# Kernel tuning notes

Hardware: AMD Instinct MI355X
Metric: run time of the kernel (lower is better)

## Reference

```python
import jax, jax.numpy as jnp
import numpy as np

B, S, H, V = 2, 2048, 1024, 32000
SDS = [64, 128, 256]
EPS = 1e-5


def _ln(x, g, b):
    m = jnp.mean(x, -1, keepdims=True)
    v = jnp.var(x, -1, keepdims=True)
    return (x - m) * jax.lax.rsqrt(v + EPS) * g + b


def _layer(x, A_log, Wb, Wc, D, Wg, bg, Wo, bo, g, be):
    # x: [B,S,H]; state dim N = A_log.shape[0]
    A = jnp.exp(A_log)
    gate = jax.nn.sigmoid(jnp.einsum('bsh,nh->bsn', x, Wg) + bg)
    Bx = jnp.einsum('bsh,nh->bsn', x, Wb)
    u = gate * Bx  # [B,S,N]

    def step(s, u_t):
        s = A * s + u_t
        return s, s

    s0 = jnp.zeros((x.shape[0], A.shape[0]), x.dtype)
    _, states = jax.lax.scan(step, s0, jnp.swapaxes(u, 0, 1))  # [S,B,N]
    states = jnp.swapaxes(states, 0, 1)
    y = jnp.einsum('bsn,hn->bsh', states, Wc) + D * x
    out = _ln(y + x, g, be)
    return out @ Wo.T + bo  # dropout is identity (p used in eval / p=0)


def setup_inputs() -> dict:
    key = jax.random.key(0)
    ks = iter(jax.random.split(key, 64))
    d = {}
    d['x'] = jax.random.randint(next(ks), (B, S), 0, V)
    d['E'] = jax.random.normal(next(ks), (V, H), jnp.float32) * 0.02
    for i, N in enumerate(SDS):
        d[f'A{i}'] = jnp.log(jnp.exp(jnp.full((N,), -0.5)) + 0.1 * jax.random.normal(next(ks), (N,)))
        d[f'Wb{i}'] = jax.random.normal(next(ks), (N, H), jnp.float32) * 0.02
        d[f'Wc{i}'] = jax.random.normal(next(ks), (H, N), jnp.float32) * 0.02
        d[f'D{i}'] = jax.random.normal(next(ks), (H,), jnp.float32)
        d[f'Wg{i}'] = jax.random.normal(next(ks), (N, H), jnp.float32) * 0.02
        d[f'bg{i}'] = jnp.zeros((N,), jnp.float32)
        d[f'Wo{i}'] = jax.random.normal(next(ks), (H, H), jnp.float32) * 0.02
        d[f'bo{i}'] = jnp.zeros((H,), jnp.float32)
        d[f'g{i}'] = jnp.ones((H,), jnp.float32)
        d[f'be{i}'] = jnp.zeros((H,), jnp.float32)
    d['Wf'] = jax.random.normal(next(ks), (H, 3 * H), jnp.float32) * 0.02
    d['bf'] = jnp.zeros((H,), jnp.float32)
    d['gf'] = jnp.ones((H,), jnp.float32)
    d['bef'] = jnp.zeros((H,), jnp.float32)
    d['Wh'] = jax.random.normal(next(ks), (V, H), jnp.float32) * 0.02
    d['bh'] = jnp.zeros((V,), jnp.float32)
    return d


def reference(x, E,
              A0, Wb0, Wc0, D0, Wg0, bg0, Wo0, bo0, g0, be0,
              A1, Wb1, Wc1, D1, Wg1, bg1, Wo1, bo1, g1, be1,
              A2, Wb2, Wc2, D2, Wg2, bg2, Wo2, bo2, g2, be2,
              Wf, bf, gf, bef, Wh, bh):
    emb = E[x]  # [B,S,H]
    o0 = _layer(emb, A0, Wb0, Wc0, D0, Wg0, bg0, Wo0, bo0, g0, be0)
    o1 = _layer(emb, A1, Wb1, Wc1, D1, Wg1, bg1, Wo1, bo1, g1, be1)
    o2 = _layer(emb, A2, Wb2, Wc2, D2, Wg2, bg2, Wo2, bo2, g2, be2)
    combined = jnp.concatenate([o0, o1, o2], axis=-1)  # [B,S,3H]
    fused = combined @ Wf.T + bf
    fused = _ln(fused + emb, gf, bef)
    logits = fused @ Wh.T + bh  # [B,S,V]
    return logits
```

## Files before the change

### kernel.cpp

```cpp
#include <hip/hip_runtime.h>
#include <hip/hip_bf16.h>

#define Hd 1024
#define Bdim 2
#define Sd 2048
#define BSd 4096
#define Vd 32000
#define EPSf 1e-5f
#define CH 16
#define NCH 128
#define NT3 448

typedef __attribute__((ext_vector_type(8))) short short8;
typedef __attribute__((ext_vector_type(4))) float f32x4;
typedef __attribute__((ext_vector_type(4))) unsigned short us4;

__device__ __forceinline__ unsigned short f2bf(float f) {
  union { float f; unsigned int u; } v; v.f = f;
  return (unsigned short)((v.u + 0x7fffu + ((v.u >> 16) & 1u)) >> 16);
}

typedef __attribute__((address_space(1))) const void gvoid_t;
typedef __attribute__((address_space(3))) void svoid_t;
__device__ __forceinline__ void gl_lds16(const void* g, void* s) {
  __builtin_amdgcn_global_load_lds((gvoid_t*)g, (svoid_t*)s, 16, 0, 0);
}

struct CvtTab {
  const float* src[11];
  unsigned short* dst[11];
  int start[12];
};
__global__ void k_cvt_all(CvtTab tab) {
  int b = blockIdx.x;
  int j = 0;
  while (j < 10 && b >= tab.start[j + 1]) ++j;
  size_t i = (size_t)(b - tab.start[j]) * 256 + threadIdx.x;
  f32x4 v = *(const f32x4*)(tab.src[j] + i * 4);
  us4 o;
  o[0] = f2bf(v[0]); o[1] = f2bf(v[1]); o[2] = f2bf(v[2]); o[3] = f2bf(v[3]);
  *(us4*)(tab.dst[j] + i * 4) = o;
}

__global__ void k_cvtT(const float* __restrict__ s0, const float* __restrict__ s1,
                       const float* __restrict__ s2, unsigned short* __restrict__ dst) {
  const float* src = blockIdx.z == 0 ? s0 : (blockIdx.z == 1 ? s1 : s2);
  unsigned short* d = dst + (size_t)blockIdx.z * Hd * Hd;
  __shared__ float tile[32][33];
  int tx = threadIdx.x & 31, ty = threadIdx.x >> 5;
  int bx = blockIdx.x * 32, by = blockIdx.y * 32;
  #pragma unroll
  for (int i = 0; i < 4; ++i)
    tile[ty + i * 8][tx] = src[(size_t)(by + ty + i * 8) * Hd + bx + tx];
  __syncthreads();
  #pragma unroll
  for (int i = 0; i < 4; ++i)
    d[(size_t)(bx + ty + i * 8) * Hd + by + tx] = f2bf(tile[tx][ty + i * 8]);
}

__global__ void k_biasf(const float* __restrict__ Wf_, const float* __restrict__ bfb,
                        const float* __restrict__ bo0, const float* __restrict__ bo1,
                        const float* __restrict__ bo2, float* __restrict__ biasf) {
  int h = blockIdx.x, t = threadIdx.x;
  float s = 0.f;
  for (int c = t; c < 3072; c += 256) {
    float b = c < 1024 ? bo0[c] : (c < 2048 ? bo1[c - 1024] : bo2[c - 2048]);
    s += Wf_[(size_t)h * 3072 + c] * b;
  }
  #pragma unroll
  for (int o = 32; o >= 1; o >>= 1) s += __shfl_xor(s, o);
  __shared__ float red[4];
  if ((t & 63) == 0) red[t >> 6] = s;
  __syncthreads();
  if (t == 0) biasf[h] = bfb[h] + red[0] + red[1] + red[2] + red[3];
}

__global__ void k_setup(const float* A0, const float* A1, const float* A2,
                        const float* b0, const float* b1, const float* b2,
                        const float* D0, const float* D1, const float* D2,
                        const float* g0, const float* g1, const float* g2,
                        const float* e0, const float* e1, const float* e2,
                        float* Alog448, float* bg448,
                        float* D3, float* g3, float* be3) {
  int t = blockIdx.x * 256 + threadIdx.x;
  if (t < NT3) {
    int l = t < 64 ? 0 : (t < 192 ? 1 : 2);
    int o = t - (l == 0 ? 0 : (l == 1 ? 64 : 192));
    Alog448[t] = (l == 0 ? A0 : (l == 1 ? A1 : A2))[o];
    bg448[t]   = (l == 0 ? b0 : (l == 1 ? b1 : b2))[o];
  }
  if (t < 3072) {
    int l = t >> 10, o = t & 1023;
    D3[t]  = (l == 0 ? D0 : (l == 1 ? D1 : D2))[o];
    g3[t]  = (l == 0 ? g0 : (l == 1 ? g1 : g2))[o];
    be3[t] = (l == 0 ? e0 : (l == 1 ? e1 : e2))[o];
  }
}

__global__ void k_embed(const int* __restrict__ x, const float* __restrict__ E,
                        float* __restrict__ emb, unsigned short* __restrict__ embbf) {
  int row = blockIdx.x, t = threadIdx.x;
  int id = x[row];
  f32x4 v = *(const f32x4*)(E + (size_t)id * Hd + t * 4);
  *(f32x4*)(emb + (size_t)row * Hd + t * 4) = v;
  us4 o;
  o[0] = f2bf(v[0]); o[1] = f2bf(v[1]); o[2] = f2bf(v[2]); o[3] = f2bf(v[3]);
  *(us4*)(embbf + (size_t)row * Hd + t * 4) = o;
}

template<int BM, int BN, int WM, int WN, int BF16_OUT>
__launch_bounds__(WM * WN * 64)
__global__ void gemm2ph(const unsigned short* __restrict__ A,
                        const unsigned short* __restrict__ Bw,
                        const float* __restrict__ bias,
                        void* __restrict__ Cv,
                        int N, int K, int lda, int ldb, int ldc, int coff, int tm)
{
  constexpr int NT = WM * WN * 64;
  constexpr int MF = BM / WM / 16;
  constexpr int NF = BN / WN / 16;
  constexpr int ASZ = BM * 64;
  constexpr int BSZ = BN * 64;
  constexpr int AR = (ASZ * 2) / (NT * 16);
  constexpr int BR = (BSZ * 2) / (NT * 16);
  __shared__ __align__(16) unsigned short Sm[2 * (ASZ + BSZ)];

  int T = gridDim.x;
  int orig = blockIdx.x;
  int q = T >> 3, r = T & 7;
  int xc = orig & 7, sdv = orig >> 3;
  int wgid = (xc < r ? xc * (q + 1) : r * (q + 1) + (xc - r) * q) + sdv;
  int n_t = wgid / tm, m_t = wgid % tm;
  int row0 = m_t * BM, col0 = n_t * BN;

  int tid = threadIdx.x;
  int wave = tid >> 6, lane = tid & 63;
  int wm = wave / WN, wn = wave % WN;
  int wr = wm * (BM / WM), wc = wn * (BN / WN);
  int lr = lane & 15;
  int klane = lane >> 4;

  f32x4 acc[MF][NF] = {};

  auto stage = [&](int buf, int k0) {
    unsigned short* Ab = Sm + buf * (ASZ + BSZ);
    unsigned short* Bb = Ab + ASZ;
    #pragma unroll
    for (int j = 0; j < AR; ++j) {
      int slot = j * NT + tid;
      int lrow = slot >> 3, c16 = slot & 7;
      int scol = (c16 ^ (lrow & 7)) * 8;
      gl_lds16(A + (size_t)(row0 + lrow) * lda + k0 + scol, Ab + (j * NT + wave * 64) * 8);
    }
    #pragma unroll
    for (int j = 0; j < BR; ++j) {
      int slot = j * NT + tid;
      int lrow = slot >> 3, c16 = slot & 7;
      int scol = (c16 ^ (lrow & 7)) * 8;
      int brow = col0 + lrow;
      if (brow >= N) brow = N - 1;
      gl_lds16(Bw + (size_t)brow * ldb + k0 + scol, Bb + (j * NT + wave * 64) * 8);
    }
  };

  auto compute = [&](int buf) {
    const unsigned short* Ab = Sm + buf * (ASZ + BSZ);
    const unsigned short* Bb = Ab + ASZ;
    #pragma unroll
    for (int kk = 0; kk < 2; ++kk) {
      short8 afr[MF], bfr[NF];
      #pragma unroll
      for (int m = 0; m < MF; ++m) {
        int row = wr + m * 16 + lr;
        int cs = (kk * 4 + klane) ^ (row & 7);
        afr[m] = *(const short8*)(Ab + row * 64 + cs * 8);
      }
      #pragma unroll
      for (int n = 0; n < NF; ++n) {
        int row = wc + n * 16 + lr;
        int cs = (kk * 4 + klane) ^ (row & 7);
        bfr[n] = *(const short8*)(Bb + row * 64 + cs * 8);
      }
      #pragma unroll
      for (int m = 0; m < MF; ++m)
        #pragma unroll
        for (int n = 0; n < NF; ++n)
          acc[m][n] = __builtin_amdgcn_mfma_f32_16x16x32_bf16(afr[m], bfr[n], acc[m][n], 0, 0, 0);
    }
  };

  int nt = K >> 6;
  stage(0, 0);
  __syncthreads();
  for (int t = 0; t < nt - 1; ++t) {
    stage((t & 1) ^ 1, (t + 1) * 64);
    compute(t & 1);
    __syncthreads();
  }
  compute((nt - 1) & 1);

  int rb = (lane >> 4) * 4;
  #pragma unroll
  for (int m = 0; m < MF; ++m) {
    #pragma unroll
    for (int n = 0; n < NF; ++n) {
      int gcol = col0 + wc + n * 16 + lr;
      if (gcol >= N) continue;
      float bv = bias ? bias[gcol] : 0.f;
      #pragma unroll
      for (int j = 0; j < 4; ++j) {
        int grow = row0 + wr + m * 16 + rb + j;
        float val = acc[m][n][j] + bv;
        if (BF16_OUT)
          ((unsigned short*)Cv)[(size_t)grow * ldc + coff + gcol] = f2bf(val);
        else
          ((float*)Cv)[(size_t)grow * ldc + coff + gcol] = val;
      }
    }
  }
}

__launch_bounds__(256)
__global__ void gemm_bd3(const unsigned short* __restrict__ Awf,
                         const unsigned short* __restrict__ Bwo,
                         unsigned short* __restrict__ Cw)
{
  constexpr int ASZ = 128 * 64, BSZ = 128 * 64;
  __shared__ __align__(16) unsigned short Sm[2 * (ASZ + BSZ)];
  int T = gridDim.x;
  int orig = blockIdx.x;
  int q = T >> 3, r = T & 7;
  int xc = orig & 7, sdv = orig >> 3;
  int wgid = (xc < r ? xc * (q + 1) : r * (q + 1) + (xc - r) * q) + sdv;
  int n_g = wgid / 8, m_t = wgid % 8;
  int li = n_g >> 3, n_t = n_g & 7;
  const unsigned short* A = Awf + li * Hd;
  const unsigned short* Bw = Bwo + ((size_t)li << 20);
  int row0 = m_t * 128, col0 = n_t * 128;

  int tid = threadIdx.x;
  int wave = tid >> 6, lane = tid & 63;
  int wm = wave >> 1, wn = wave & 1;
  int wr = wm * 64, wc = wn * 64;
  int lr = lane & 15, klane = lane >> 4;

  f32x4 acc[4][4] = {};
  auto stage = [&](int buf, int k0) {
    unsigned short* Ab = Sm + buf * (ASZ + BSZ);
    unsigned short* Bb = Ab + ASZ;
    #pragma unroll
    for (int j = 0; j < 4; ++j) {
      int slot = j * 256 + tid;
      int lrow = slot >> 3, c16 = slot & 7;
      int scol = (c16 ^ (lrow & 7)) * 8;
      gl_lds16(A + (size_t)(row0 + lrow) * 3072 + k0 + scol, Ab + (j * 256 + wave * 64) * 8);
      gl_lds16(Bw + (size_t)(col0 + lrow) * 1024 + k0 + scol, Bb + (j * 256 + wave * 64) * 8);
    }
  };
  auto compute = [&](int buf) {
    const unsigned short* Ab = Sm + buf * (ASZ + BSZ);
    const unsigned short* Bb = Ab + ASZ;
    #pragma unroll
    for (int kk = 0; kk < 2; ++kk) {
      short8 afr[4], bfr[4];
      #pragma unroll
      for (int m = 0; m < 4; ++m) {
        int row = wr + m * 16 + lr;
        int cs = (kk * 4 + klane) ^ (row & 7);
        afr[m] = *(const short8*)(Ab + row * 64 + cs * 8);
      }
      #pragma unroll
      for (int n = 0; n < 4; ++n) {
        int row = wc + n * 16 + lr;
        int cs = (kk * 4 + klane) ^ (row & 7);
        bfr[n] = *(const short8*)(Bb + row * 64 + cs * 8);
      }
      #pragma unroll
      for (int m = 0; m < 4; ++m)
        #pragma unroll
        for (int n = 0; n < 4; ++n)
          acc[m][n] = __builtin_amdgcn_mfma_f32_16x16x32_bf16(afr[m], bfr[n], acc[m][n], 0, 0, 0);
    }
  };
  stage(0, 0);
  __syncthreads();
  for (int t = 0; t < 15; ++t) {
    stage((t & 1) ^ 1, (t + 1) * 64);
    compute(t & 1);
    __syncthreads();
  }
  compute(1);

  int rb = (lane >> 4) * 4;
  #pragma unroll
  for (int m = 0; m < 4; ++m)
    #pragma unroll
    for (int n = 0; n < 4; ++n) {
      int gcol = li * Hd + col0 + wc + n * 16 + lr;
      #pragma unroll
      for (int j = 0; j < 4; ++j) {
        int grow = row0 + wr + m * 16 + rb + j;
        Cw[(size_t)grow * 3072 + gcol] = f2bf(acc[m][n][j]);
      }
    }
}

__launch_bounds__(512)
__global__ void gemm8ph(const unsigned short* __restrict__ A,
                        const unsigned short* __restrict__ Bw,
                        const float* __restrict__ bias,
                        float* __restrict__ Cv,
                        int N, int K, int lda, int ldb, int ldc, int tm)
{
  __shared__ __align__(16) unsigned short Sm[65536];

  int T = gridDim.x;
  int orig = blockIdx.x;
  int q = T >> 3, r = T & 7;
  int xc = orig & 7, sdv = orig >> 3;
  int wgid = (xc < r ? xc * (q + 1) : r * (q + 1) + (xc - r) * q) + sdv;
  int n_t = wgid / tm, m_t = wgid % tm;
  int row0 = m_t * 256, col0 = n_t * 256;

  int tid = threadIdx.x;
  int wave = tid >> 6, lane = tid & 63;
  int wm = wave >> 2, wn = wave & 3;
  int lr = lane & 15, klane = lane >> 4;

  f32x4 acc[8][4] = {};

  auto stageA = [&](int b, int h, int kt) {
    unsigned short* base = Sm + (b * 2 + h) * 8192;
    #pragma unroll
    for (int j = 0; j < 2; ++j) {
      int slot = j * 512 + tid;
      int lrow = slot >> 3, c16 = slot & 7;
      int scol = (c16 ^ (lrow & 7)) * 8;
      gl_lds16(A + (size_t)(row0 + h * 128 + lrow) * lda + kt * 64 + scol,
               base + (j * 512 + wave * 64) * 8);
    }
  };
  auto stageB = [&](int b, int h, int kt) {
    unsigned short* base = Sm + 32768 + (b * 2 + h) * 8192;
    #pragma unroll
    for (int j = 0; j < 2; ++j) {
      int slot = j * 512 + tid;
      int lrow = slot >> 3, c16 = slot & 7;
      int scol = (c16 ^ (lrow & 7)) * 8;
      gl_lds16(Bw + (size_t)(col0 + h * 128 + lrow) * ldb + kt * 64 + scol,
               base + (j * 512 + wave * 64) * 8);
    }
  };
  auto readA = [&](short8* afr, int b, int mh, int kk) {
    const unsigned short* base = Sm + (b * 2 + mh) * 8192;
    #pragma unroll
    for (int f = 0; f < 4; ++f) {
      int rowin = f * 32 + wm * 16 + lr;
      int cs = (kk * 4 + klane) ^ (rowin & 7);
      afr[f] = *(const short8*)(base + rowin * 64 + cs * 8);
    }
  };
  auto readB = [&](short8* bfr, int b, int kk) {
    #pragma unroll
    for (int n = 0; n < 4; ++n) {
      int rowin = (n & 1) * 64 + wn * 16 + lr;
      const unsigned short* base = Sm + 32768 + (b * 2 + (n >> 1)) * 8192;
      int cs = (kk * 4 + klane) ^ (rowin & 7);
      bfr[n] = *(const short8*)(base + rowin * 64 + cs * 8);
    }
  };

  #define MFMA16(mh, afr, bfr)                                                  \
    __builtin_amdgcn_s_setprio(1);                                              \
    _Pragma("unroll")                                                           \
    for (int f = 0; f < 4; ++f)                                                 \
      _Pragma("unroll")                                                         \
      for (int n = 0; n < 4; ++n)                                               \
        acc[(mh) * 4 + f][n] = __builtin_amdgcn_mfma_f32_16x16x32_bf16(         \
            bfr[n], afr[f], acc[(mh) * 4 + f][n], 0, 0, 0);                     \
    __builtin_amdgcn_s_setprio(0);

  #define BAR()   __builtin_amdgcn_s_barrier()
  #define FEN()   asm volatile("" ::: "memory")
  #define VM4()   asm volatile("s_waitcnt vmcnt(4)" ::: "memory")
  #define VM0()   asm volatile("s_waitcnt vmcnt(0)" ::: "memory")

  int nt = K >> 6;
  int iters = K >> 7;

  stageA(0, 0, 0); stageB(0, 0, 0); stageB(0, 1, 0); stageA(0, 1, 0);
  stageA(1, 0, 1); stageB(1, 0, 1);
  VM4(); BAR();

  short8 afr[4], bfr0[4], bfr1[4];
  for (int i = 0; i < iters; ++i) {
    int t1 = 2 * i + 1, t2 = 2 * i + 2, t3 = 2 * i + 3;
    bool last = (i == iters - 1);
    readA(afr, 0, 0, 0); readB(bfr0, 0, 0);
    BAR(); FEN();
    stageB(1, 1, t1); stageA(1, 1, t1);
    MFMA16(0, afr, bfr0);
    BAR();
    readA(afr, 0, 0, 1); readB(bfr1, 0, 1);
    BAR(); FEN();
    MFMA16(0, afr, bfr1);
    BAR();
    readA(afr, 0, 1, 0);
    BAR(); FEN();
    if (t2 < nt) stageA(0, 0, t2);
    MFMA16(1, afr, bfr0);
    BAR();
    readA(afr, 0, 1, 1);
    BAR(); FEN();
    if (t2 < nt) stageB(0, 0, t2);
    MFMA16(1, afr, bfr1);
    if (last) { VM0(); } else { VM4(); }
    BAR();
    readA(afr, 1, 0, 0); readB(bfr0, 1, 0);
    BAR(); FEN();
    if (t2 < nt) { stageB(0, 1, t2); stageA(0, 1, t2); }
    MFMA16(0, afr, bfr0);
    BAR();
    readA(afr, 1, 0, 1); readB(bfr1, 1, 1);
    BAR(); FEN();
    MFMA16(0, afr, bfr1);
    BAR();
    readA(afr, 1, 1, 0);
    BAR(); FEN();
    if (t3 < nt) stageA(1, 0, t3);
    MFMA16(1, afr, bfr0);
    BAR();
    readA(afr, 1, 1, 1);
    BAR(); FEN();
    if (t3 < nt) stageB(1, 0, t3);
    MFMA16(1, afr, bfr1);
    if (!last) { VM4(); }
    BAR();
  }

  int cb = klane * 4;
  #pragma unroll
  for (int idx = 0; idx < 8; ++idx) {
    int mh = idx >> 2, f = idx & 3;
    int grow = row0 + mh * 128 + f * 32 + wm * 16 + lr;
    float* crow = Cv + (size_t)grow * ldc;
    #pragma unroll
    for (int n = 0; n < 4; ++n) {
      int gcol = col0 + (n & 1) * 64 + (n >> 1) * 128 + wn * 16 + cb;
      f32x4 bv = *(const f32x4*)(bias + gcol);
      f32x4 o;
      o[0] = acc[idx][n][0] + bv[0];
      o[1] = acc[idx][n][1] + bv[1];
      o[2] = acc[idx][n][2] + bv[2];
      o[3] = acc[idx][n][3] + bv[3];
      *(f32x4*)(crow + gcol) = o;
    }
  }
  #undef MFMA16
  #undef BAR
  #undef FEN
  #undef VM4
  #undef VM0
}

__global__ void k_scanA(const float* __restrict__ gzbx, const float* __restrict__ Alog448,
                        const float* __restrict__ bg448,
                        float* __restrict__ st, float* __restrict__ carry) {
  int gid = blockIdx.x * 256 + threadIdx.x;
  if (gid >= Bdim * NCH * NT3) return;
  int n = gid % NT3;
  int c = (gid / NT3) % NCH;
  int b = gid / (NT3 * NCH);
  float a = expf(Alog448[n]);
  float bgv = bg448[n];
  float s = 0.f;
  size_t rbase = (size_t)b * Sd + (size_t)c * CH;
  for (int t = 0; t < CH; ++t) {
    size_t row = rbase + t;
    float gzv = gzbx[row * 896 + n];
    float bxv = gzbx[row * 896 + 448 + n];
    float gv = 1.f / (1.f + expf(-(gzv + bgv)));
    s = a * s + gv * bxv;
    st[row * NT3 + n] = s;
  }
  carry[((size_t)b * NCH + c) * NT3 + n] = s;
}

__global__ void k_scanB(const float* __restrict__ carry, const float* __restrict__ Alog448,
                        float* __restrict__ cin) {
  int i = blockIdx.x * 256 + threadIdx.x;
  if (i >= Bdim * NT3) return;
  int b = i / NT3, n = i % NT3;
  float aC = expf((float)CH * Alog448[n]);
  float s = 0.f;
  for (int c = 0; c < NCH; ++c) {
    cin[((size_t)b * NCH + c) * NT3 + n] = s;
    s = aC * s + carry[((size_t)b * NCH + c) * NT3 + n];
  }
}

__global__ void k_scanC(const float* __restrict__ st, const float* __restrict__ cin,
                        const float* __restrict__ Alog448, unsigned short* __restrict__ stbf) {
  size_t gid = (size_t)blockIdx.x * 256 + threadIdx.x;
  if (gid >= (size_t)BSd * NT3) return;
  int n = gid % NT3;
  int row = gid / NT3;
  int b = row / Sd, sg = row % Sd;
  int c = sg / CH, t = sg % CH;
  float cv = cin[((size_t)b * NCH + c) * NT3 + n];
  float val = st[gid] + expf((float)(t + 1) * Alog448[n]) * cv;
  stbf[gid] = f2bf(val);
}

__global__ void k_ln3(const float* __restrict__ y3, const float* __restrict__ emb,
                      const float* __restrict__ D3, const float* __restrict__ g3,
                      const float* __restrict__ be3, unsigned short* __restrict__ z3) {
  int row = blockIdx.x, ly = blockIdx.y, t = threadIdx.x;
  const float* y = y3 + (size_t)row * 3072 + ly * 1024;
  f32x4 yv = *(const f32x4*)(y + t * 4);
  f32x4 ev = *(const f32x4*)(emb + (size_t)row * Hd + t * 4);
  float vals[4];
  float sum = 0.f, sq = 0.f;
  #pragma unroll
  for (int j = 0; j < 4; ++j) {
    float coef = D3[ly * 1024 + t * 4 + j] + 1.f;
    float v = yv[j] + coef * ev[j];
    vals[j] = v; sum += v; sq += v * v;
  }
  #pragma unroll
  for (int o = 32; o >= 1; o >>= 1) {
    sum += __shfl_xor(sum, o);
    sq += __shfl_xor(sq, o);
  }
  __shared__ float red[2][4];
  int w = t >> 6, lane = t & 63;
  if (lane == 0) { red[0][w] = sum; red[1][w] = sq; }
  __syncthreads();
  sum = red[0][0] + red[0][1] + red[0][2] + red[0][3];
  sq  = red[1][0] + red[1][1] + red[1][2] + red[1][3];
  float mean = sum * (1.f / Hd);
  float var = sq * (1.f / Hd) - mean * mean;
  float rs = rsqrtf(var + EPSf);
  us4 o4;
  #pragma unroll
  for (int j = 0; j < 4; ++j) {
    float z = (vals[j] - mean) * rs * g3[ly * 1024 + t * 4 + j] + be3[ly * 1024 + t * 4 + j];
    o4[j] = f2bf(z);
  }
  *(us4*)(z3 + (size_t)row * 3072 + ly * 1024 + t * 4) = o4;
}

__global__ void k_ln(const float* __restrict__ y, const float* __restrict__ emb,
                     const float* __restrict__ g, const float* __restrict__ be,
                     unsigned short* __restrict__ out) {
  int row = blockIdx.x, t = threadIdx.x;
  f32x4 yv = *(const f32x4*)(y + (size_t)row * Hd + t * 4);
  f32x4 ev = *(const f32x4*)(emb + (size_t)row * Hd + t * 4);
  float vals[4];
  float sum = 0.f, sq = 0.f;
  #pragma unroll
  for (int j = 0; j < 4; ++j) {
    float v = yv[j] + ev[j];
    vals[j] = v; sum += v; sq += v * v;
  }
  #pragma unroll
  for (int o = 32; o >= 1; o >>= 1) {
    sum += __shfl_xor(sum, o);
    sq += __shfl_xor(sq, o);
  }
  __shared__ float red[2][4];
  int w = t >> 6, lane = t & 63;
  if (lane == 0) { red[0][w] = sum; red[1][w] = sq; }
  __syncthreads();
  sum = red[0][0] + red[0][1] + red[0][2] + red[0][3];
  sq  = red[1][0] + red[1][1] + red[1][2] + red[1][3];
  float mean = sum * (1.f / Hd);
  float var = sq * (1.f / Hd) - mean * mean;
  float rs = rsqrtf(var + EPSf);
  us4 o4;
  #pragma unroll
  for (int j = 0; j < 4; ++j) {
    float z = (vals[j] - mean) * rs * g[t * 4 + j] + be[t * 4 + j];
    o4[j] = f2bf(z);
  }
  *(us4*)(out + (size_t)row * Hd + t * 4) = o4;
}

extern "C" void kernel_launch(void* const* d_in, const int* in_sizes, int n_in,
                              void* d_out, int out_size, void* d_ws, size_t ws_size,
                              hipStream_t stream) {
  (void)in_sizes; (void)n_in; (void)out_size; (void)ws_size;
  const int* x = (const int*)d_in[0];
  const float* E = (const float*)d_in[1];
  const float* Wf_ = (const float*)d_in[32];
  const float* bfb = (const float*)d_in[33];
  const float* gfp = (const float*)d_in[34];
  const float* bef = (const float*)d_in[35];
  const float* Wh_ = (const float*)d_in[36];
  const float* bh = (const float*)d_in[37];

  char* wsb = (char*)d_ws;
  size_t off = 0;
  auto alloc = [&](size_t bytes) -> void* {
    void* p = wsb + off;
    off += (bytes + 255) & ~(size_t)255;
    return p;
  };
  float* emb             = (float*)alloc((size_t)BSd * Hd * 4);
  unsigned short* embbf  = (unsigned short*)alloc((size_t)BSd * Hd * 2);
  unsigned short* wgwbbf = (unsigned short*)alloc((size_t)896 * Hd * 2);
  unsigned short* wcbf   = (unsigned short*)alloc((size_t)NT3 * Hd * 2);
  unsigned short* wotbf  = (unsigned short*)alloc((size_t)3 * Hd * Hd * 2);
  unsigned short* wfbf   = (unsigned short*)alloc((size_t)3 * Hd * Hd * 2);
  unsigned short* wcombbf= (unsigned short*)alloc((size_t)Hd * 3 * Hd * 2);
  unsigned short* whbf   = (unsigned short*)alloc((size_t)Vd * Hd * 2);
  float* gzbx            = (float*)alloc((size_t)BSd * 896 * 4);
  float* stl             = (float*)alloc((size_t)BSd * NT3 * 4);
  unsigned short* stbf   = (unsigned short*)alloc((size_t)BSd * NT3 * 2);
  float* carry           = (float*)alloc((size_t)Bdim * NCH * NT3 * 4);
  float* cin             = (float*)alloc((size_t)Bdim * NCH * NT3 * 4);
  float* ybuf3           = (float*)alloc((size_t)BSd * 3072 * 4);
  unsigned short* zbf3   = (unsigned short*)alloc((size_t)BSd * 3072 * 2);
  unsigned short* zbf    = (unsigned short*)alloc((size_t)BSd * Hd * 2);
  float* Alog448         = (float*)alloc(NT3 * 4);
  float* bg448           = (float*)alloc(NT3 * 4);
  float* D3              = (float*)alloc(3072 * 4);
  float* g3              = (float*)alloc(3072 * 4);
  float* be3             = (float*)alloc(3072 * 4);
  float* biasf           = (float*)alloc(Hd * 4);

  k_embed<<<BSd, 256, 0, stream>>>(x, E, emb, embbf);

  {
    CvtTab tab;
    const int rowoff_g[3] = {0, 64, 192};
    int j = 0;
    int n4s[11];
    for (int i = 0; i < 3; ++i) { tab.src[j] = (const float*)d_in[2 + 10 * i + 4]; tab.dst[j] = wgwbbf + (size_t)rowoff_g[i] * Hd;         n4s[j] = (64 << i) * Hd / 4; ++j; }
    for (int i = 0; i < 3; ++i) { tab.src[j] = (const float*)d_in[2 + 10 * i + 1]; tab.dst[j] = wgwbbf + (size_t)(448 + rowoff_g[i]) * Hd;  n4s[j] = (64 << i) * Hd / 4; ++j; }
    for (int i = 0; i < 3; ++i) { tab.src[j] = (const float*)d_in[2 + 10 * i + 2]; tab.dst[j] = wcbf + (size_t)rowoff_g[i] * Hd;            n4s[j] = (64 << i) * Hd / 4; ++j; }
    tab.src[j] = Wf_; tab.dst[j] = wfbf; n4s[j] = 3 * Hd * Hd / 4; ++j;
    tab.src[j] = Wh_; tab.dst[j] = whbf; n4s[j] = Vd * Hd / 4; ++j;
    tab.start[0] = 0;
    for (int k = 0; k < 11; ++k) tab.start[k + 1] = tab.start[k] + (n4s[k] + 255) / 256;
    k_cvt_all<<<tab.start[11], 256, 0, stream>>>(tab);
  }

  k_cvtT<<<dim3(32, 32, 3), 256, 0, stream>>>(
      (const float*)d_in[8], (const float*)d_in[18], (const float*)d_in[28], wotbf);

  k_setup<<<12, 256, 0, stream>>>(
      (const float*)d_in[2], (const float*)d_in[12], (const float*)d_in[22],
      (const float*)d_in[7], (const float*)d_in[17], (const float*)d_in[27],
      (const float*)d_in[5], (const float*)d_in[15], (const float*)d_in[25],
      (const float*)d_in[10], (const float*)d_in[20], (const float*)d_in[30],
      (const float*)d_in[11], (const float*)d_in[21], (const float*)d_in[31],
      Alog448, bg448, D3, g3, be3);

  k_biasf<<<Hd, 256, 0, stream>>>(Wf_, bfb,
      (const float*)d_in[9], (const float*)d_in[19], (const float*)d_in[29], biasf);

  gemm_bd3<<<192, 256, 0, stream>>>(wfbf, wotbf, wcombbf);

  const int TM = BSd / 128;

  gemm2ph<128,128,2,2,0><<<(896 / 128) * TM, 256, 0, stream>>>(
      embbf, wgwbbf, nullptr, gzbx, 896, Hd, Hd, Hd, 896, 0, TM);

  {
    int totA = Bdim * NCH * NT3;
    k_scanA<<<(totA + 255) / 256, 256, 0, stream>>>(gzbx, Alog448, bg448, stl, carry);
    k_scanB<<<(Bdim * NT3 + 255) / 256, 256, 0, stream>>>(carry, Alog448, cin);
    size_t totC = (size_t)BSd * NT3;
    k_scanC<<<(int)((totC + 255) / 256), 256, 0, stream>>>(stl, cin, Alog448, stbf);
  }

  const int owg[3] = {0, 64, 192};
  const int sd[3] = {64, 128, 256};
  for (int i = 0; i < 3; ++i) {
    gemm2ph<128,128,2,2,0><<<(Hd / 128) * TM, 256, 0, stream>>>(
        stbf + owg[i], wcbf + (size_t)owg[i] * Hd, nullptr, ybuf3,
        Hd, sd[i], NT3, sd[i], 3072, i * Hd, TM);
  }

  k_ln3<<<dim3(BSd, 3), 256, 0, stream>>>(ybuf3, emb, D3, g3, be3, zbf3);

  gemm2ph<128,128,2,2,0><<<(Hd / 128) * TM, 256, 0, stream>>>(
      zbf3, wcombbf, biasf, ybuf3, Hd, 3 * Hd, 3 * Hd, 3 * Hd, Hd, 0, TM);
  k_ln<<<BSd, 256, 0, stream>>>(ybuf3, emb, gfp, bef, zbf);

  const int TM256 = BSd / 256;
  gemm8ph<<<(Vd / 256) * TM256, 512, 0, stream>>>(
      zbf, whbf, bh, (float*)d_out, Vd, Hd, Hd, Hd, Vd, TM256);
}
```

Baseline: 616.7 us.

## Merge three Wc GEMMs into one launch and reorder LM-head tile traversal

Replaces the three per-layer state-to-hidden GEMM launches with a single kernel, gemm_wc3, that interleaves tiles from all three layers, each with its own K (64/128/256). This cuts launch overhead and lets the small-K work fill the GPU together. The vocab GEMM now walks tiles row-major (M-tile outer, N-tile inner) and swaps the MFMA operand order. Its output store changes from 16-byte vector writes to scalar per-row writes, which may reduce store efficiency on the large logits output.

```diff
diff --git a/kernel.cpp b/kernel.cpp
--- a/kernel.cpp
+++ b/kernel.cpp
@@ -218,6 +218,95 @@
       }
     }
   }
+}
+
+__launch_bounds__(256)
+__global__ void gemm_wc3(const unsigned short* __restrict__ St,
+                         const unsigned short* __restrict__ Wc,
+                         float* __restrict__ Cv)
+{
+  constexpr int ASZ = 128 * 64, BSZ = 128 * 64;
+  __shared__ __align__(16) unsigned short Sm[2 * (ASZ + BSZ)];
+  int T = gridDim.x;
+  int orig = blockIdx.x;
+  int q = T >> 3, r = T & 7;
+  int xc = orig & 7, sdv = orig >> 3;
+  int wgid = (xc < r ? xc * (q + 1) : r * (q + 1) + (xc - r) * q) + sdv;
+  int l = wgid % 3;
+  int w2 = wgid / 3;
+  int n_t = w2 >> 5, m_t = w2 & 31;
+  const int owgl = l == 0 ? 0 : (l == 1 ? 64 : 192);
+  const int K = 64 << l;
+  const unsigned short* A = St + owgl;
+  const unsigned short* Bw = Wc + (size_t)owgl * Hd;
+  int row0 = m_t * 128, col0 = n_t * 128;
+
+  int tid = threadIdx.x;
+  int wave = tid >> 6, lane = tid & 63;
+  int wm = wave >> 1, wn = wave & 1;
+  int wr = wm * 64, wc = wn * 64;
+  int lr = lane & 15, klane = lane >> 4;
+
+  f32x4 acc[4][4] = {};
+  auto stage = [&](int buf, int k0) {
+    unsigned short* Ab = Sm + buf * (ASZ + BSZ);
+    unsigned short* Bb = Ab + ASZ;
+    #pragma unroll
+    for (int j = 0; j < 4; ++j) {
+      int slot = j * 256 + tid;
+      int lrow = slot >> 3, c16 = slot & 7;
+      int scol = (c16 ^ (lrow & 7)) * 8;
+      gl_lds16(A + (size_t)(row0 + lrow) * NT3 + k0 + scol, Ab + (j * 256 + wave * 64) * 8);
+      gl_lds16(Bw + (size_t)(col0 + lrow) * K + k0 + scol, Bb + (j * 256 + wave * 64) * 8);
+    }
+  };
+  auto compute = [&](int buf) {
+    const unsigned short* Ab = Sm + buf * (ASZ + BSZ);
+    const unsigned short* Bb = Ab + ASZ;
+    #pragma unroll
+    for (int kk = 0; kk < 2; ++kk) {
+      short8 afr[4], bfr[4];
+      #pragma unroll
+      for (int m = 0; m < 4; ++m) {
+        int row = wr + m * 16 + lr;
+        int cs = (kk * 4 + klane) ^ (row & 7);
+        afr[m] = *(const short8*)(Ab + row * 64 + cs * 8);
+      }
+      #pragma unroll
+      for (int n = 0; n < 4; ++n) {
+        int row = wc + n * 16 + lr;
+        int cs = (kk * 4 + klane) ^ (row & 7);
+        bfr[n] = *(const short8*)(Bb + row * 64 + cs * 8);
+      }
+      #pragma unroll
+      for (int m = 0; m < 4; ++m)
+        #pragma unroll
+        for (int n = 0; n < 4; ++n)
+          acc[m][n] = __builtin_amdgcn_mfma_f32_16x16x32_bf16(afr[m], bfr[n], acc[m][n], 0, 0, 0);
+    }
+  };
+  int nt = K >> 6;
+  stage(0, 0);
+  __syncthreads();
+  for (int t = 0; t < nt - 1; ++t) {
+    stage((t & 1) ^ 1, (t + 1) * 64);
+    compute(t & 1);
+    __syncthreads();
+  }
+  compute((nt - 1) & 1);
+
+  int rb = (lane >> 4) * 4;
+  #pragma unroll
+  for (int m = 0; m < 4; ++m)
+    #pragma unroll
+    for (int n = 0; n < 4; ++n) {
+      int gcol = l * Hd + col0 + wc + n * 16 + lr;
+      #pragma unroll
+      for (int j = 0; j < 4; ++j) {
+        int grow = row0 + wr + m * 16 + rb + j;
+        Cv[(size_t)grow * 3072 + gcol] = acc[m][n][j];
+      }
+    }
 }
 
 __launch_bounds__(256)
@@ -310,7 +399,7 @@
                         const unsigned short* __restrict__ Bw,
                         const float* __restrict__ bias,
                         float* __restrict__ Cv,
-                        int N, int K, int lda, int ldb, int ldc, int tm)
+                        int N, int K, int lda, int ldb, int ldc, int tn)
 {
   __shared__ __align__(16) unsigned short Sm[65536];
 
@@ -319,7 +408,7 @@
   int q = T >> 3, r = T & 7;
   int xc = orig & 7, sdv = orig >> 3;
   int wgid = (xc < r ? xc * (q + 1) : r * (q + 1) + (xc - r) * q) + sdv;
-  int n_t = wgid / tm, m_t = wgid % tm;
+  int m_t = wgid / tn, n_t = wgid % tn;
   int row0 = m_t * 256, col0 = n_t * 256;
 
   int tid = threadIdx.x;
@@ -377,7 +466,7 @@
       _Pragma("unroll")                                                         \
       for (int n = 0; n < 4; ++n)                                               \
         acc[(mh) * 4 + f][n] = __builtin_amdgcn_mfma_f32_16x16x32_bf16(         \
-            bfr[n], afr[f], acc[(mh) * 4 + f][n], 0, 0, 0);                     \
+            afr[f], bfr[n], acc[(mh) * 4 + f][n], 0, 0, 0);                     \
     __builtin_amdgcn_s_setprio(0);
 
   #define BAR()   __builtin_amdgcn_s_barrier()
@@ -438,22 +527,18 @@
     BAR();
   }
 
-  int cb = klane * 4;
+  int rb = (lane >> 4) * 4;
   #pragma unroll
   for (int idx = 0; idx < 8; ++idx) {
     int mh = idx >> 2, f = idx & 3;
-    int grow = row0 + mh * 128 + f * 32 + wm * 16 + lr;
-    float* crow = Cv + (size_t)grow * ldc;
+    int growb = row0 + mh * 128 + f * 32 + wm * 16 + rb;
     #pragma unroll
     for (int n = 0; n < 4; ++n) {
-      int gcol = col0 + (n & 1) * 64 + (n >> 1) * 128 + wn * 16 + cb;
-      f32x4 bv = *(const f32x4*)(bias + gcol);
-      f32x4 o;
-      o[0] = acc[idx][n][0] + bv[0];
-      o[1] = acc[idx][n][1] + bv[1];
-      o[2] = acc[idx][n][2] + bv[2];
-      o[3] = acc[idx][n][3] + bv[3];
-      *(f32x4*)(crow + gcol) = o;
+      int gcol = col0 + (n & 1) * 64 + (n >> 1) * 128 + wn * 16 + lr;
+      float bv = bias[gcol];
+      #pragma unroll
+      for (int j = 0; j < 4; ++j)
+        Cv[(size_t)(growb + j) * ldc + gcol] = acc[idx][n][j] + bv;
     }
   }
   #undef MFMA16
@@ -675,13 +760,7 @@
     k_scanC<<<(int)((totC + 255) / 256), 256, 0, stream>>>(stl, cin, Alog448, stbf);
   }
 
-  const int owg[3] = {0, 64, 192};
-  const int sd[3] = {64, 128, 256};
-  for (int i = 0; i < 3; ++i) {
-    gemm2ph<128,128,2,2,0><<<(Hd / 128) * TM, 256, 0, stream>>>(
-        stbf + owg[i], wcbf + (size_t)owg[i] * Hd, nullptr, ybuf3,
-        Hd, sd[i], NT3, sd[i], 3072, i * Hd, TM);
-  }
+  gemm_wc3<<<768, 256, 0, stream>>>(stbf, wcbf, ybuf3);
 
   k_ln3<<<dim3(BSd, 3), 256, 0, stream>>>(ybuf3, emb, D3, g3, be3, zbf3);
 
@@ -689,7 +768,7 @@
       zbf3, wcombbf, biasf, ybuf3, Hd, 3 * Hd, 3 * Hd, 3 * Hd, Hd, 0, TM);
   k_ln<<<BSd, 256, 0, stream>>>(ybuf3, emb, gfp, bef, zbf);
 
-  const int TM256 = BSd / 256;
-  gemm8ph<<<(Vd / 256) * TM256, 512, 0, stream>>>(
-      zbf, whbf, bh, (float*)d_out, Vd, Hd, Hd, Hd, Vd, TM256);
-}
+  const int TN = Vd / 256;
+  gemm8ph<<<(BSd / 256) * TN, 512, 0, stream>>>(
+      zbf, whbf, bh, (float*)d_out, Vd, Hd, Hd, Hd, Vd, TN);
+}
```

Result: faster. 560.0 us (-9.2%).
